# Kernel tuning notes

Measured on AMD Instinct MI355X. Metric: run time of the kernel, lower is better.

## Reference

```python
import jax, jax.numpy as jnp
import numpy as np

B, M, D = 16, 100000, 128
OUT = 128  # out_features; in_features = 2*D


def setup_inputs() -> dict:
    key = jax.random.key(0)
    k1, k2, k3, k4 = jax.random.split(key, 4)
    s1 = 1.0 / np.sqrt(2 * D)  # ~ torch Linear default init scale
    s2 = 1.0 / np.sqrt(OUT)
    return {
        "xx_anchor": jax.random.normal(k1, (B, D), dtype=jnp.float32),
        "input": jax.random.normal(k2, (M, D), dtype=jnp.float32),
        "adj": jnp.zeros((1, 1), dtype=jnp.float32),  # densified then unused in forward math
        "W1": jax.random.normal(k3, (OUT, 2 * D), dtype=jnp.float32) * s1,
        "W2": jax.random.normal(k4, (1, OUT), dtype=jnp.float32) * s2,
    }


def reference(xx_anchor, input, adj, W1, W2):
    d = input.shape[1]
    # concat(q_vec, input) @ W1.T  ==  q @ W1[:, :d].T  +  input @ W1[:, d:].T
    # (avoids materializing the [B, m, 2d] concat tensor; same math)
    anchor_part = xx_anchor @ W1[:, :d].T          # [B, out]
    node_part = input @ W1[:, d:].T                # [m, out]
    h = jax.nn.relu(anchor_part[:, None, :] + node_part[None, :, :])  # [B, m, out]
    scores = jnp.einsum('bmo,o->bm', h, W2[0])     # linear2 -> [B, m]
    atten = jax.nn.softmax(scores, axis=1)          # softmax over node dim
    v_vec = jnp.einsum('bm,md->bd', atten, input)   # weighted sum pooling
    return v_vec
```

## Files before the change

kernel.cpp:

```cpp
#include <hip/hip_runtime.h>
#include <hip/hip_bf16.h>
#include <math.h>


typedef __attribute__((ext_vector_type(8))) short bf16x8;
typedef __attribute__((ext_vector_type(4))) float f32x4;

__device__ __forceinline__ short f2bs(float f) {
    __hip_bfloat16 h = __float2bfloat16(f);
    return *reinterpret_cast<short*>(&h);
}
__device__ __forceinline__ float bs2f(ushort u) {
    union { unsigned int i; float f; } v; v.i = ((unsigned)u) << 16; return v.f;
}
__device__ __forceinline__ bf16x8 pack8(float4 a, float4 b) {
    bf16x8 r;
    r[0] = f2bs(a.x); r[1] = f2bs(a.y); r[2] = f2bs(a.z); r[3] = f2bs(a.w);
    r[4] = f2bs(b.x); r[5] = f2bs(b.y); r[6] = f2bs(b.z); r[7] = f2bs(b.w);
    return r;
}

__global__ __launch_bounds__(256) void kA(const float* __restrict__ W1,
                                          const float* __restrict__ xx,
                                          ushort* __restrict__ w1b,
                                          float* __restrict__ A) {
    const int bi = blockIdx.x, t = threadIdx.x;
    if (bi < 64) {
        int idx = bi * 256 + t;
        int o = idx >> 7, d = idx & 127;
        w1b[idx] = (ushort)f2bs(W1[o * 256 + 128 + d]);
        return;
    }
    __shared__ float xxs[16 * 132];
    __shared__ float w1s[16 * 132];
    const int og0 = (bi - 64) * 16;
#pragma unroll
    for (int i = 0; i < 2; ++i) {
        int idx = t + 256 * i;
        int r = idx >> 5, c4 = (idx & 31) << 2;
        *(float4*)&xxs[r * 132 + c4] = *(const float4*)&xx[r * 128 + c4];
        *(float4*)&w1s[r * 132 + c4] = *(const float4*)&W1[(og0 + r) * 256 + c4];
    }
    __syncthreads();
    const int ol = t >> 4, b = t & 15;
    float acc = 0.f;
#pragma unroll
    for (int d4 = 0; d4 < 32; ++d4) {
        float4 xv = *(float4*)&xxs[b * 132 + d4 * 4];
        float4 wv = *(float4*)&w1s[ol * 132 + d4 * 4];
        acc += xv.x * wv.x + xv.y * wv.y + xv.z * wv.z + xv.w * wv.w;
    }
    A[b * 128 + og0 + ol] = acc;
}

__global__ __launch_bounds__(256, 3) void kB(
    const float* __restrict__ in, const ushort* __restrict__ w1b,
    const float* __restrict__ W2, const float* __restrict__ A,
    float* __restrict__ lsum_g, ushort* __restrict__ pacc, int M) {
    __shared__ ushort ins[128 * 136];
    __shared__ float As[16 * 128];
    __shared__ ushort pb[16 * 136];

    const int tid = threadIdx.x, bid = blockIdx.x;
    const int m0 = bid * 128;
    const int w = tid >> 6, lane = tid & 63;
    const int c = lane & 15, q = lane >> 4;
    const int lim = (M - m0 < 128) ? (M - m0) : 128;

#pragma unroll
    for (int i = 0; i < 2; ++i) {
        int idx = tid + 256 * i;
        *(float4*)&As[idx * 4] = *(const float4*)&A[idx * 4];
    }

    const int r0 = w * 32 + c;
    const int r1 = r0 + 16;
    const bool v0 = r0 < lim, v1 = r1 < lim;
    const float* __restrict__ row0 = in + (size_t)(m0 + r0) * 128;
    const float* __restrict__ row1 = in + (size_t)(m0 + r1) * 128;

    f32x4 acc[2][8];
#pragma unroll
    for (int mt = 0; mt < 2; ++mt)
#pragma unroll
        for (int ot = 0; ot < 8; ++ot) acc[mt][ot] = (f32x4){0.f, 0.f, 0.f, 0.f};
#pragma unroll
    for (int kb = 0; kb < 4; ++kb) {
        const int k0 = kb * 32 + q * 8;
        float4 a0 = make_float4(0.f, 0.f, 0.f, 0.f), a1 = a0, b0 = a0, b1 = a0;
        if (v0) { a0 = *(const float4*)&row0[k0]; a1 = *(const float4*)&row0[k0 + 4]; }
        if (v1) { b0 = *(const float4*)&row1[k0]; b1 = *(const float4*)&row1[k0 + 4]; }
        bf16x8 bv0 = pack8(a0, a1);
        bf16x8 bv1 = pack8(b0, b1);
        *(bf16x8*)&ins[r0 * 136 + k0] = bv0;
        *(bf16x8*)&ins[r1 * 136 + k0] = bv1;
#pragma unroll
        for (int ot = 0; ot < 8; ++ot) {
            bf16x8 av = *(const bf16x8*)(w1b + (ot * 16 + c) * 128 + k0);
            acc[0][ot] = __builtin_amdgcn_mfma_f32_16x16x32_bf16(av, bv0, acc[0][ot], 0, 0, 0);
            acc[1][ot] = __builtin_amdgcn_mfma_f32_16x16x32_bf16(av, bv1, acc[1][ot], 0, 0, 0);
        }
    }

    f32x4 w2q[8];
#pragma unroll
    for (int ot = 0; ot < 8; ++ot) {
        f32x4 wv = *(const f32x4*)&W2[ot * 16 + q * 4];
        w2q[ot] = wv * 0.5f;
    }
    __syncthreads();

    float sm0 = 0.f, sm1 = 0.f;
#pragma unroll
    for (int ot = 0; ot < 8; ++ot)
#pragma unroll
        for (int r = 0; r < 4; ++r) {
            sm0 += acc[0][ot][r] * w2q[ot][r];
            sm1 += acc[1][ot][r] * w2q[ot][r];
        }

#pragma unroll
    for (int b = 0; b < 16; ++b) {
        float sa0 = sm0, sa1 = sm1, sb0 = 0.f, sb1 = 0.f;
#pragma unroll
        for (int ot = 0; ot < 8; ot += 2) {
            f32x4 aq0 = *(f32x4*)&As[b * 128 + ot * 16 + q * 4];
            f32x4 aq1 = *(f32x4*)&As[b * 128 + (ot + 1) * 16 + q * 4];
#pragma unroll
            for (int r = 0; r < 4; ++r) {
                sa0 += fabsf(acc[0][ot][r]     + aq0[r]) * w2q[ot][r];
                sa1 += fabsf(acc[1][ot][r]     + aq0[r]) * w2q[ot][r];
                sb0 += fabsf(acc[0][ot + 1][r] + aq1[r]) * w2q[ot + 1][r];
                sb1 += fabsf(acc[1][ot + 1][r] + aq1[r]) * w2q[ot + 1][r];
            }
        }
        float s0 = sa0 + sb0, s1 = sa1 + sb1;
        s0 += __shfl_xor(s0, 16, 64);
        s0 += __shfl_xor(s0, 32, 64);
        s1 += __shfl_xor(s1, 16, 64);
        s1 += __shfl_xor(s1, 32, 64);
        if (q == (b & 3)) {
            pb[b * 136 + r0] = (ushort)f2bs(v0 ? __expf(s0) : 0.f);
            pb[b * 136 + r1] = (ushort)f2bs(v1 ? __expf(s1) : 0.f);
        }
    }
    __syncthreads();

    f32x4 pd[2];
    pd[0] = (f32x4){0.f, 0.f, 0.f, 0.f};
    pd[1] = (f32x4){0.f, 0.f, 0.f, 0.f};
#pragma unroll
    for (int ks = 0; ks < 4; ++ks) {
        bf16x8 pf = *(const bf16x8*)&pb[c * 136 + ks * 32 + q * 8];
#pragma unroll
        for (int t = 0; t < 2; ++t) {
            const int dloc = w * 32 + t * 16 + c;
            bf16x8 bf;
#pragma unroll
            for (int j = 0; j < 8; ++j)
                bf[j] = (short)ins[(ks * 32 + q * 8 + j) * 136 + dloc];
            pd[t] = __builtin_amdgcn_mfma_f32_16x16x32_bf16(pf, bf, pd[t], 0, 0, 0);
        }
    }
#pragma unroll
    for (int t = 0; t < 2; ++t)
#pragma unroll
        for (int r = 0; r < 4; ++r)
            pacc[((size_t)bid * 16 + q * 4 + r) * 128 + w * 32 + t * 16 + c] =
                (ushort)f2bs(pd[t][r]);

    {
        const int bb = tid >> 4, jj = tid & 15;
        const ushort* pr = &pb[bb * 136 + jj * 8];
        float part = 0.f;
#pragma unroll
        for (int j2 = 0; j2 < 8; ++j2) part += bs2f(pr[j2]);
#pragma unroll
        for (int off = 1; off < 16; off <<= 1) part += __shfl_xor(part, off, 64);
        if (jj == 0) lsum_g[bid * 16 + bb] = part;
    }
}

__global__ __launch_bounds__(256) void kC1(
    const float* __restrict__ lsum_g, const ushort* __restrict__ pacc,
    float* __restrict__ pacc2, float* __restrict__ lsum2, int nb) {
    const int b = blockIdx.x >> 4, s = blockIdx.x & 15;
    const int t = threadIdx.x;
    __shared__ float reda[2 * 128];
    __shared__ float redl[2];
    const int cs = (nb + 15) >> 4;
    const int blk0 = s * cs;
    int blk1 = blk0 + cs; if (blk1 > nb) blk1 = nb;
    const int dd = t & 127, h = t >> 7;
    float ac = 0.f, ls = 0.f;
    for (int blk = blk0 + h; blk < blk1; blk += 2) {
        ac += bs2f(pacc[((size_t)blk * 16 + b) * 128 + dd]);
        ls += lsum_g[blk * 16 + b];
    }
    reda[h * 128 + dd] = ac;
    if (dd == 0) redl[h] = ls;
    __syncthreads();
    if (h == 0) {
        pacc2[((size_t)s * 16 + b) * 128 + dd] = reda[dd] + reda[128 + dd];
        if (dd == 0) lsum2[s * 16 + b] = redl[0] + redl[1];
    }
}

__global__ void kFin(const float* __restrict__ pacc2, const float* __restrict__ lsum2,
                     float* __restrict__ out) {
    const int b = blockIdx.x, t = threadIdx.x;
    float ac = 0.f, ls = 0.f;
#pragma unroll
    for (int s = 0; s < 16; ++s) {
        ac += pacc2[((size_t)s * 16 + b) * 128 + t];
        ls += lsum2[s * 16 + b];
    }
    out[b * 128 + t] = ac / ls;
}

extern "C" void kernel_launch(void* const* d_in, const int* in_sizes, int n_in,
                              void* d_out, int out_size, void* d_ws, size_t ws_size,
                              hipStream_t stream) {
    const float* xx = (const float*)d_in[0];
    const float* in = (const float*)d_in[1];
    const float* W1 = (const float*)d_in[3];
    const float* W2 = (const float*)d_in[4];
    float* out = (float*)d_out;

    const int M = in_sizes[1] / 128;
    const int nb = (M + 127) / 128;

    float* ws = (float*)d_ws;
    float* A      = ws;
    float* lsum_g = A + 2048;
    float* pacc2  = lsum_g + (size_t)nb * 16;
    float* lsum2  = pacc2 + 256 * 128;
    ushort* w1b   = (ushort*)(lsum2 + 256);
    ushort* pacc  = w1b + 16384;

    kA  <<<72, 256, 0, stream>>>(W1, xx, w1b, A);
    kB  <<<nb, 256, 0, stream>>>(in, w1b, W2, A, lsum_g, pacc, M);
    kC1 <<<256, 256, 0, stream>>>(lsum_g, pacc, pacc2, lsum2, nb);
    kFin<<<16, 128, 0, stream>>>(pacc2, lsum2, out);
}
```

Baseline: 137.6 us.

## Prefetch all input row loads upfront and fold final reduction into kC1 via atomics

In kB, all 16 float4 loads of both input rows are issued at kernel start, before the A staging and the MFMA loop. Out-of-range rows are clamped to the last row instead of branched on, so the loads can overlap instead of being serialized per k-block. The kFin launch is removed: kC1 now atomically accumulates into zero-initialised buffers (zeroed by an extra kA block), and the last block, found through an atomic counter, computes the output. This trades one kernel launch for atomics and higher register pressure in kB. Clamped rows still get zero weight because their probabilities are masked by v0/v1.

Result: slower. 181.5 us (+32.0%).

```diff
diff --git a/kernel.cpp b/kernel.cpp
--- a/kernel.cpp
+++ b/kernel.cpp
@@ -23,12 +23,21 @@
 __global__ __launch_bounds__(256) void kA(const float* __restrict__ W1,
                                           const float* __restrict__ xx,
                                           ushort* __restrict__ w1b,
-                                          float* __restrict__ A) {
+                                          float* __restrict__ A,
+                                          float* __restrict__ acc2,
+                                          float* __restrict__ lsum2,
+                                          int* __restrict__ counter) {
     const int bi = blockIdx.x, t = threadIdx.x;
     if (bi < 64) {
         int idx = bi * 256 + t;
         int o = idx >> 7, d = idx & 127;
         w1b[idx] = (ushort)f2bs(W1[o * 256 + 128 + d]);
+        return;
+    }
+    if (bi == 72) {
+        for (int i = t; i < 2048; i += 256) acc2[i] = 0.f;
+        if (t < 16) lsum2[t] = 0.f;
+        if (t == 0) *counter = 0;
         return;
     }
     __shared__ float xxs[16 * 132];
@@ -67,40 +76,55 @@
     const int c = lane & 15, q = lane >> 4;
     const int lim = (M - m0 < 128) ? (M - m0) : 128;
 
+    const int r0 = w * 32 + c;
+    const int r1 = r0 + 16;
+    const bool v0 = r0 < lim, v1 = r1 < lim;
+    int cr0 = m0 + r0; if (cr0 > M - 1) cr0 = M - 1;
+    int cr1 = m0 + r1; if (cr1 > M - 1) cr1 = M - 1;
+    const float* __restrict__ row0 = in + (size_t)cr0 * 128;
+    const float* __restrict__ row1 = in + (size_t)cr1 * 128;
+
+    const int kq = q * 8;
+    float4 pA0 = *(const float4*)&row0[kq];       float4 pA1 = *(const float4*)&row0[kq + 4];
+    float4 pB0 = *(const float4*)&row0[kq + 32];  float4 pB1 = *(const float4*)&row0[kq + 36];
+    float4 pC0 = *(const float4*)&row0[kq + 64];  float4 pC1 = *(const float4*)&row0[kq + 68];
+    float4 pD0 = *(const float4*)&row0[kq + 96];  float4 pD1 = *(const float4*)&row0[kq + 100];
+    float4 qA0 = *(const float4*)&row1[kq];       float4 qA1 = *(const float4*)&row1[kq + 4];
+    float4 qB0 = *(const float4*)&row1[kq + 32];  float4 qB1 = *(const float4*)&row1[kq + 36];
+    float4 qC0 = *(const float4*)&row1[kq + 64];  float4 qC1 = *(const float4*)&row1[kq + 68];
+    float4 qD0 = *(const float4*)&row1[kq + 96];  float4 qD1 = *(const float4*)&row1[kq + 100];
+
 #pragma unroll
     for (int i = 0; i < 2; ++i) {
         int idx = tid + 256 * i;
         *(float4*)&As[idx * 4] = *(const float4*)&A[idx * 4];
     }
 
-    const int r0 = w * 32 + c;
-    const int r1 = r0 + 16;
-    const bool v0 = r0 < lim, v1 = r1 < lim;
-    const float* __restrict__ row0 = in + (size_t)(m0 + r0) * 128;
-    const float* __restrict__ row1 = in + (size_t)(m0 + r1) * 128;
-
     f32x4 acc[2][8];
 #pragma unroll
     for (int mt = 0; mt < 2; ++mt)
 #pragma unroll
         for (int ot = 0; ot < 8; ++ot) acc[mt][ot] = (f32x4){0.f, 0.f, 0.f, 0.f};
-#pragma unroll
-    for (int kb = 0; kb < 4; ++kb) {
-        const int k0 = kb * 32 + q * 8;
-        float4 a0 = make_float4(0.f, 0.f, 0.f, 0.f), a1 = a0, b0 = a0, b1 = a0;
-        if (v0) { a0 = *(const float4*)&row0[k0]; a1 = *(const float4*)&row0[k0 + 4]; }
-        if (v1) { b0 = *(const float4*)&row1[k0]; b1 = *(const float4*)&row1[k0 + 4]; }
-        bf16x8 bv0 = pack8(a0, a1);
-        bf16x8 bv1 = pack8(b0, b1);
-        *(bf16x8*)&ins[r0 * 136 + k0] = bv0;
-        *(bf16x8*)&ins[r1 * 136 + k0] = bv1;
-#pragma unroll
-        for (int ot = 0; ot < 8; ++ot) {
-            bf16x8 av = *(const bf16x8*)(w1b + (ot * 16 + c) * 128 + k0);
-            acc[0][ot] = __builtin_amdgcn_mfma_f32_16x16x32_bf16(av, bv0, acc[0][ot], 0, 0, 0);
-            acc[1][ot] = __builtin_amdgcn_mfma_f32_16x16x32_bf16(av, bv1, acc[1][ot], 0, 0, 0);
-        }
-    }
+
+#define NP_STEP(kb, Pa, Pb, Qa, Qb)                                               \
+    {                                                                             \
+        const int k0 = (kb) * 32 + kq;                                            \
+        bf16x8 bv0 = pack8(Pa, Pb);                                               \
+        bf16x8 bv1 = pack8(Qa, Qb);                                               \
+        *(bf16x8*)&ins[r0 * 136 + k0] = bv0;                                      \
+        *(bf16x8*)&ins[r1 * 136 + k0] = bv1;                                      \
+        _Pragma("unroll")                                                         \
+        for (int ot = 0; ot < 8; ++ot) {                                          \
+            bf16x8 av = *(const bf16x8*)(w1b + (ot * 16 + c) * 128 + k0);         \
+            acc[0][ot] = __builtin_amdgcn_mfma_f32_16x16x32_bf16(av, bv0, acc[0][ot], 0, 0, 0); \
+            acc[1][ot] = __builtin_amdgcn_mfma_f32_16x16x32_bf16(av, bv1, acc[1][ot], 0, 0, 0); \
+        }                                                                         \
+    }
+    NP_STEP(0, pA0, pA1, qA0, qA1)
+    NP_STEP(1, pB0, pB1, qB0, qB1)
+    NP_STEP(2, pC0, pC1, qC0, qC1)
+    NP_STEP(3, pD0, pD1, qD0, qD1)
+#undef NP_STEP
 
     f32x4 w2q[8];
 #pragma unroll
@@ -183,7 +207,8 @@
 
 __global__ __launch_bounds__(256) void kC1(
     const float* __restrict__ lsum_g, const ushort* __restrict__ pacc,
-    float* __restrict__ pacc2, float* __restrict__ lsum2, int nb) {
+    float* __restrict__ acc2, float* __restrict__ lsum2,
+    int* __restrict__ counter, float* __restrict__ out, int nb) {
     const int b = blockIdx.x >> 4, s = blockIdx.x & 15;
     const int t = threadIdx.x;
     __shared__ float reda[2 * 128];
@@ -201,21 +226,21 @@
     if (dd == 0) redl[h] = ls;
     __syncthreads();
     if (h == 0) {
-        pacc2[((size_t)s * 16 + b) * 128 + dd] = reda[dd] + reda[128 + dd];
-        if (dd == 0) lsum2[s * 16 + b] = redl[0] + redl[1];
-    }
-}
-
-__global__ void kFin(const float* __restrict__ pacc2, const float* __restrict__ lsum2,
-                     float* __restrict__ out) {
-    const int b = blockIdx.x, t = threadIdx.x;
-    float ac = 0.f, ls = 0.f;
-#pragma unroll
-    for (int s = 0; s < 16; ++s) {
-        ac += pacc2[((size_t)s * 16 + b) * 128 + t];
-        ls += lsum2[s * 16 + b];
-    }
-    out[b * 128 + t] = ac / ls;
+        atomicAdd(&acc2[b * 128 + dd], reda[dd] + reda[128 + dd]);
+        if (dd == 0) atomicAdd(&lsum2[b], redl[0] + redl[1]);
+    }
+
+    __threadfence();
+    __shared__ int isLast;
+    if (t == 0) isLast = (atomicAdd(counter, 1) == 255);
+    __syncthreads();
+    if (isLast) {
+        for (int i = t; i < 2048; i += 256) {
+            float a = atomicAdd(&acc2[i], 0.f);
+            float l = atomicAdd(&lsum2[i >> 7], 0.f);
+            out[i] = a / l;
+        }
+    }
 }
 
 extern "C" void kernel_launch(void* const* d_in, const int* in_sizes, int n_in,
@@ -231,15 +256,15 @@
     const int nb = (M + 127) / 128;
 
     float* ws = (float*)d_ws;
-    float* A      = ws;
-    float* lsum_g = A + 2048;
-    float* pacc2  = lsum_g + (size_t)nb * 16;
-    float* lsum2  = pacc2 + 256 * 128;
-    ushort* w1b   = (ushort*)(lsum2 + 256);
-    ushort* pacc  = w1b + 16384;
-
-    kA  <<<72, 256, 0, stream>>>(W1, xx, w1b, A);
+    float* A       = ws;
+    float* acc2    = A + 2048;
+    float* lsum2   = acc2 + 2048;
+    int*   counter = (int*)(lsum2 + 16);
+    float* lsum_g  = (float*)(counter + 16);
+    ushort* w1b    = (ushort*)(lsum_g + (size_t)nb * 16);
+    ushort* pacc   = w1b + 16384;
+
+    kA  <<<73, 256, 0, stream>>>(W1, xx, w1b, A, acc2, lsum2, counter);
     kB  <<<nb, 256, 0, stream>>>(in, w1b, W2, A, lsum_g, pacc, M);
-    kC1 <<<256, 256, 0, stream>>>(lsum_g, pacc, pacc2, lsum2, nb);
-    kFin<<<16, 128, 0, stream>>>(pacc2, lsum2, out);
-}
+    kC1 <<<256, 256, 0, stream>>>(lsum_g, pacc, acc2, lsum2, counter, out, nb);
+}
```
